# Optimization experiments

Hardware: AMD Instinct MI355X
Metric: run time of the kernel (lower is better)

Reference implementation:

```python
import jax, jax.numpy as jnp
import numpy as np
import math

NHEADS = 8


def pos_encoding_2d(d_model, H, W):
    dm = d_model // 2
    div = jnp.exp(jnp.arange(0, dm, 2, dtype=jnp.float32) * (-math.log(10000.0) / dm))  # [dm//2]
    pw = jnp.arange(W, dtype=jnp.float32)[:, None] * div  # [W, dm//2]
    ph = jnp.arange(H, dtype=jnp.float32)[:, None] * div  # [H, dm//2]
    pe = jnp.zeros((d_model, H, W), jnp.float32)
    pe = pe.at[0:dm:2].set(jnp.broadcast_to(jnp.sin(pw).T[:, None, :], (dm // 2, H, W)))
    pe = pe.at[1:dm:2].set(jnp.broadcast_to(jnp.cos(pw).T[:, None, :], (dm // 2, H, W)))
    pe = pe.at[dm::2].set(jnp.broadcast_to(jnp.sin(ph).T[:, :, None], (dm // 2, H, W)))
    pe = pe.at[dm + 1::2].set(jnp.broadcast_to(jnp.cos(ph).T[:, :, None], (dm // 2, H, W)))
    return pe


def conv_same(x, w, b):
    y = jax.lax.conv_general_dilated(x, w, (1, 1), 'SAME',
                                     dimension_numbers=('NCHW', 'OIHW', 'NCHW'))
    return y + b[None, :, None, None]


def layernorm(x, g, b, eps=1e-5):
    mu = x.mean(-1, keepdims=True)
    var = ((x - mu) ** 2).mean(-1, keepdims=True)
    return (x - mu) / jnp.sqrt(var + eps) * g + b


def setup_inputs() -> dict:
    key = jax.random.key(0)
    B, C, H, W = 8, 256, 32, 32
    KQV, NH, K = 64, NHEADS, 3
    ks = jax.random.split(key, 16)
    s_conv = 1.0 / math.sqrt(C * K * K)
    s_lin = 1.0 / math.sqrt(NH * KQV)
    s_ff = 1.0 / math.sqrt(C)
    return {
        'x': jax.random.normal(ks[0], (B, C, H, W), jnp.float32),
        'Wk': jax.random.normal(ks[1], (NH * KQV, C, K, K), jnp.float32) * s_conv,
        'bk': jax.random.normal(ks[2], (NH * KQV,), jnp.float32) * s_conv,
        'Wq': jax.random.normal(ks[3], (NH * KQV, C, K, K), jnp.float32) * s_conv,
        'bq': jax.random.normal(ks[4], (NH * KQV,), jnp.float32) * s_conv,
        'Wv': jax.random.normal(ks[5], (NH * KQV, C, K, K), jnp.float32) * s_conv,
        'bv': jax.random.normal(ks[6], (NH * KQV,), jnp.float32) * s_conv,
        'Wproj': jax.random.normal(ks[7], (C, NH * KQV), jnp.float32) * s_lin,
        'bproj': jax.random.normal(ks[8], (C,), jnp.float32) * s_lin,
        'ln_g': jnp.ones((C,), jnp.float32),
        'ln_b': jnp.zeros((C,), jnp.float32),
        'W1': jax.random.normal(ks[9], (C, C), jnp.float32) * s_ff,
        'b1': jax.random.normal(ks[10], (C,), jnp.float32) * s_ff,
        'W2': jax.random.normal(ks[11], (C, C), jnp.float32) * s_ff,
        'b2': jax.random.normal(ks[12], (C,), jnp.float32) * s_ff,
    }


def reference(x, Wk, bk, Wq, bq, Wv, bv, Wproj, bproj, ln_g, ln_b, W1, b1, W2, b2):
    B, C, H, W = x.shape
    N = H * W
    pe = pos_encoding_2d(C, H, W)
    xp = x + pe[None]                                   # [B,C,H,W]
    xflat = xp.reshape(B, C, N).transpose(0, 2, 1)      # [B,N,C]

    def heads(w, b):
        return conv_same(xp, w, b).reshape(B, NHEADS, -1, N)  # [B,h,c,N]

    k = heads(Wk, bk)
    q = heads(Wq, bq)
    v = heads(Wv, bv)
    scores = jnp.einsum('bhcn,bhcm->bhnm', k, q) / N    # K^T Q / N, [B,h,N,N]
    sm = jax.nn.softmax(scores, axis=1)                 # Softmax2d -> over HEAD dim (faithful)
    att = jnp.einsum('bhnm,bhcm->bhnc', sm, v)          # [B,h,N,c]
    att = att.transpose(0, 2, 3, 1).reshape(B, N, -1)   # [B,N,c*h] (channel-major, head-minor)
    attproj = att @ Wproj.T + bproj                     # [B,N,C]
    addnormed = layernorm(xflat + attproj, ln_g, ln_b)
    h1 = addnormed @ W1.T + b1
    h1 = jnp.where(h1 > 0, h1, 0.1 * h1)                # LeakyReLU(0.1)
    h2 = h1 @ W2.T + b2
    out = layernorm(h2 + addnormed, ln_g, ln_b)         # same LN params reused (faithful)
    return out.transpose(0, 2, 1).reshape(B, C, H, W)
```

## Files before the change

### kernel.cpp

```cpp
#include <hip/hip_runtime.h>
#include <stdint.h>

typedef __attribute__((ext_vector_type(8))) short short8;
typedef __attribute__((ext_vector_type(4))) short s16x4;
typedef __attribute__((ext_vector_type(4))) float f32x4;

#define DEVI __device__ __forceinline__

#if __has_builtin(__builtin_amdgcn_mfma_f32_16x16x16_bf16)
#define MFMA16(a, b, c) __builtin_amdgcn_mfma_f32_16x16x16_bf16(a, b, c, 0, 0, 0)
#else
#define MFMA16(a, b, c) __builtin_amdgcn_mfma_f32_16x16x16bf16_1k(a, b, c, 0, 0, 0)
#endif

DEVI unsigned short f2bf(float f) {
  union { float f; uint32_t u; } v; v.f = f;
  return (unsigned short)((v.u + 0x7fffu + ((v.u >> 16) & 1u)) >> 16);
}

DEVI float bf2f(uint32_t hi16) {
  union { uint32_t u; float f; } v; v.u = hi16;
  return v.f;
}

DEVI uint32_t pkbf(float a, float b) {
  union { float f; uint32_t u; } x, y; x.f = a; y.f = b;
  return ((x.u + 0x8000u) >> 16) | (((y.u + 0x8000u) >> 16) << 16);
}

DEVI void gload_lds16(const void* g, void* l) {
  __builtin_amdgcn_global_load_lds(
      (const __attribute__((address_space(1))) uint32_t*)g,
      (__attribute__((address_space(3))) uint32_t*)l, 16, 0, 0);
}

__global__ __launch_bounds__(256) void k_xpt(const float* __restrict__ x,
                                             const float* __restrict__ T,
                                             unsigned short* __restrict__ xpt_bf,
                                             float* __restrict__ xpt_f) {
  __shared__ __align__(16) float tile[32][36];
  const int b = blockIdx.z, c0 = blockIdx.x * 32, n0 = blockIdx.y * 32;
  const int t = threadIdx.x;
  {
    const int cl = t >> 3, ng = (t & 7) * 4;
    const int c = c0 + cl;
    float4 v = *(const float4*)(x + ((size_t)b * 256 + c) * 1024 + n0 + ng);
    float p0, p1, p2, p3;
    if (c < 128) {
      p0 = T[c * 32 + ng + 0]; p1 = T[c * 32 + ng + 1];
      p2 = T[c * 32 + ng + 2]; p3 = T[c * 32 + ng + 3];
    } else {
      p0 = p1 = p2 = p3 = T[c * 32 + (n0 >> 5)];
    }
    tile[ng + 0][cl] = v.x + p0;
    tile[ng + 1][cl] = v.y + p1;
    tile[ng + 2][cl] = v.z + p2;
    tile[ng + 3][cl] = v.w + p3;
  }
  __syncthreads();
  {
    const int nl = t >> 3, cg = (t & 7) * 4;
    float o0 = tile[nl][cg + 0], o1 = tile[nl][cg + 1];
    float o2 = tile[nl][cg + 2], o3 = tile[nl][cg + 3];
    size_t row = (size_t)b * 1024 + n0 + nl;
    *(float4*)(xpt_f + row * 256 + c0 + cg) = make_float4(o0, o1, o2, o3);
    uint32_t lo = (uint32_t)f2bf(o0) | ((uint32_t)f2bf(o1) << 16);
    uint32_t hi = (uint32_t)f2bf(o2) | ((uint32_t)f2bf(o3) << 16);
    *(uint2*)(xpt_bf + row * 256 + c0 + cg) = make_uint2(lo, hi);
  }
}

__global__ void k_prep(const float* __restrict__ Wk, const float* __restrict__ Wq,
                       const float* __restrict__ Wv, const float* __restrict__ bk,
                       const float* __restrict__ bq, const float* __restrict__ bv,
                       const float* __restrict__ Wproj, const float* __restrict__ W1,
                       const float* __restrict__ W2, unsigned short* __restrict__ Wpack,
                       float* __restrict__ bias_kqv, unsigned short* __restrict__ WprojP,
                       unsigned short* __restrict__ W1b, unsigned short* __restrict__ W2b,
                       float* __restrict__ T, float* __restrict__ zp) {
  int bid = blockIdx.x;
  if (bid < 13824) {
    int i = bid * 256 + threadIdx.x;
    if (i >= 1536 * 2304) return;
    int o = i / 2304, kn = i % 2304;
    int ci = kn & 255, khw = kn >> 8;
    const float* src = (o < 512) ? Wk : ((o < 1024) ? Wq : Wv);
    int oo = o & 511;
    Wpack[i] = f2bf(src[((size_t)oo * 256 + ci) * 9 + khw]);
  } else if (bid < 14336) {
    int i = (bid - 13824) * 256 + threadIdx.x;
    if (i < 1536)
      bias_kqv[i] = (i < 512) ? bk[i] : ((i < 1024) ? bq[i - 512] : bv[i - 1024]);
    {
      int j = i >> 9, f = i & 511;
      int h = f >> 6, c = f & 63;
      unsigned short v = f2bf(Wproj[(size_t)j * 512 + c * 8 + h]);
      WprojP[(size_t)j * 1024 + f] = v;
      WprojP[(size_t)j * 1024 + 512 + f] = v;
    }
    if (i < 65536) {
      W1b[i] = f2bf(W1[i]);
      W2b[i] = f2bf(W2[i]);
    }
  } else {
    int c = threadIdx.x;
    zp[c] = 0.0f;
    int idx = ((c >= 128) ? c - 128 : c) >> 1;
    float freq = expf(-(float)idx * (logf(10000.0f) / 64.0f));
    for (int p = 0; p < 32; ++p) {
      float ang = (float)p * freq;
      T[c * 32 + p] = (c & 1) ? cosf(ang) : sinf(ang);
    }
  }
}

__global__ __launch_bounds__(256, 2) void k_gemm_conv(const unsigned short* __restrict__ xpt,
                                                      const unsigned short* __restrict__ Wp,
                                                      unsigned short* __restrict__ kqv,
                                                      const float* __restrict__ bias,
                                                      const char* __restrict__ zp) {
  __shared__ __align__(16) unsigned short As[2][128 * 64];
  __shared__ __align__(16) unsigned short Bs[2][192 * 64];
  const int tid = threadIdx.x, l = tid & 63, w = tid >> 6;
  const int wm = w >> 1, wn = w & 1, g = l >> 4, ln = l & 15;
  const int id = blockIdx.x + (blockIdx.y << 6);
  const int nid = ((id & 7) << 6) + (id >> 3);
  const int m0 = (nid & 63) * 128, n0 = (nid >> 6) * 192;
  const int swz = (l & 7) ^ (l >> 3);

  const char* pAbase[4];
#pragma unroll
  for (int j = 0; j < 4; ++j) {
    int r = m0 + (w * 4 + j) * 8 + (l >> 3);
    pAbase[j] = (const char*)xpt + ((size_t)r * 256 + swz * 8) * 2;
  }
  const char* pB0 = (const char*)Wp +
                    ((size_t)(n0 + w * 48 + (l >> 3)) * 2304 + swz * 8) * 2;

  f32x4 acc[4][6] = {};
  int vmask = 0;
  int aoff = 0;

  auto setTap = [&](int tap) {
    int d3 = (tap * 11) >> 5;
    int dy = d3 - 1, dx = tap - d3 * 3 - 1;
    aoff = (dy * 32 + dx) * 512;
    int m = 0;
#pragma unroll
    for (int j = 0; j < 4; ++j) {
      int r = m0 + (w * 4 + j) * 8 + (l >> 3);
      int y = ((r >> 5) & 31) + dy;
      int x = (r & 31) + dx;
      if (((unsigned)y < 32u) && ((unsigned)x < 32u)) m |= (1 << j);
    }
    vmask = m;
  };

  auto STAGE = [&](int buf, int kb) {
#pragma unroll
    for (int j = 0; j < 4; ++j) {
      const char* a = (vmask & (1 << j)) ? (pAbase[j] + aoff) : zp;
      gload_lds16(a, (char*)As + buf * 16384 + (w * 4 + j) * 1024);
    }
#pragma unroll
    for (int j = 0; j < 6; ++j) {
      gload_lds16(pB0 + j * 36864 + kb, (char*)Bs + buf * 24576 + (w * 6 + j) * 1024);
    }
  };

  auto COMPUTE = [&](int buf) {
    const char* Ab2 = (const char*)As + buf * 16384;
    const char* Bb2 = (const char*)Bs + buf * 24576;
#pragma unroll
    for (int kk = 0; kk < 2; ++kk) {
      short8 af[4], bfr[6];
#pragma unroll
      for (int fm = 0; fm < 4; ++fm)
        af[fm] = *(const short8*)(Ab2 + (wm * 64 + fm * 16 + ln) * 128 +
                                  (((kk * 4 + g) ^ (ln & 7)) * 16));
#pragma unroll
      for (int fn = 0; fn < 6; ++fn)
        bfr[fn] = *(const short8*)(Bb2 + (wn * 96 + fn * 16 + ln) * 128 +
                                   (((kk * 4 + g) ^ (ln & 7)) * 16));
#pragma unroll
      for (int fm = 0; fm < 4; ++fm)
#pragma unroll
        for (int fn = 0; fn < 6; ++fn)
          acc[fm][fn] = __builtin_amdgcn_mfma_f32_16x16x32_bf16(af[fm], bfr[fn], acc[fm][fn], 0, 0, 0);
    }
  };

  setTap(0);
  STAGE(0, 0);
  aoff += 128;
  int kb = 128;
  for (int s = 0; s < 36; ++s) {
    const int buf = s & 1;
    if (s < 35) {
      if (((s + 1) & 3) == 0) setTap((s + 1) >> 2);
      STAGE(buf ^ 1, kb);
      kb += 128;
      aoff += 128;
      asm volatile("s_waitcnt vmcnt(10)" ::: "memory");
    } else {
      asm volatile("s_waitcnt vmcnt(0)" ::: "memory");
    }
    __builtin_amdgcn_s_barrier();
    __builtin_amdgcn_sched_barrier(0);
    COMPUTE(buf);
    asm volatile("s_waitcnt lgkmcnt(0)" ::: "memory");
    __builtin_amdgcn_s_barrier();
    __builtin_amdgcn_sched_barrier(0);
  }

#pragma unroll
  for (int fm = 0; fm < 4; ++fm)
#pragma unroll
    for (int fn = 0; fn < 6; ++fn) {
      int col = n0 + wn * 96 + fn * 16 + ln;
      float bb = bias[col];
#pragma unroll
      for (int r = 0; r < 4; ++r) {
        int row = m0 + wm * 64 + fm * 16 + g * 4 + r;
        kqv[(size_t)row * 1536 + col] = f2bf(acc[fm][fn][r] + bb);
      }
    }
}

__global__ __launch_bounds__(512, 4) void k_attn(const unsigned short* __restrict__ kqv,
                                                 unsigned short* __restrict__ part) {
  __shared__ __align__(16) unsigned short Qs[16][512];
  __shared__ __align__(16) char VsRaw[2][32 * 544];
  __shared__ __align__(16) float sums[4][2][64][4];
  const int tid = threadIdx.x, l = tid & 63, w = tid >> 6;
  const int g = l >> 4, ln = l & 15;
  const int nt = w & 1, hg = w >> 1;
  const int id = blockIdx.x;
  const int b = id & 7, ng = (id >> 3) & 31, ch = id >> 8;
  const int n0 = ng * 32 + nt * 16;
  const int m_base = ch * 512;
  const size_t rowBase = (size_t)b * 1024;
  const float SC = 1.0f / 1024.0f;

  short8 ak[2][2];
#pragma unroll
  for (int hl = 0; hl < 2; ++hl)
#pragma unroll
    for (int kk = 0; kk < 2; ++kk)
      ak[hl][kk] = *(const short8*)&kqv[(rowBase + n0 + ln) * 1536 +
                                        (hg * 2 + hl) * 64 + kk * 32 + g * 8];

  f32x4 acc[2][4] = {};

  const int r0 = w * 2, r1 = w * 2 + 1;
  const char* pRow = (const char*)kqv +
                     (size_t)(rowBase + m_base + r0) * 3072 + 1024 + (size_t)l * 16;
  uint4 q0, q1, v0, v1;

  auto LOADREGS = [&]() {
    q0 = *(const uint4*)pRow;
    v0 = *(const uint4*)(pRow + 1024);
    q1 = *(const uint4*)(pRow + 3072);
    v1 = *(const uint4*)(pRow + 4096);
    pRow += 49152;
  };
  char* const dQ0 = (char*)Qs + r0 * 1024 + ((l ^ (r0 & 7)) * 16);
  char* const dQ1 = (char*)Qs + r1 * 1024 + ((l ^ (r1 & 7)) * 16);
  const uint32_t vOff = (uint32_t)(l >> 1) * 544 + (uint32_t)(l & 1) * 16;
  auto DSW = [&](int vbuf) {
    *(uint4*)dQ0 = q0;
    *(uint4*)dQ1 = q1;
    char* vb = VsRaw[vbuf];
    *(uint4*)(vb + vOff + r0 * 32) = v0;
    *(uint4*)(vb + vOff + r1 * 32) = v1;
  };

  LOADREGS();
  asm volatile("s_waitcnt vmcnt(0)" ::: "memory");
  DSW(0);
  asm volatile("s_waitcnt lgkmcnt(0)" ::: "memory");
  __builtin_amdgcn_s_barrier();
  __builtin_amdgcn_sched_barrier(0);

  for (int s = 0; s < 32; ++s) {
    const int buf = s & 1;
    if (s < 31) LOADREGS();

    f32x4 sv[2] = {};
    __builtin_amdgcn_s_setprio(1);
#pragma unroll
    for (int kk = 0; kk < 2; ++kk)
#pragma unroll
      for (int hl = 0; hl < 2; ++hl) {
        int chq = (hg * 2 + hl) * 8 + kk * 4 + g;
        short8 qa = *(const short8*)((const char*)Qs + ln * 1024 +
                                     ((chq ^ (ln & 7)) * 16));
        sv[hl] = __builtin_amdgcn_mfma_f32_16x16x32_bf16(qa, ak[hl][kk], sv[hl], 0, 0, 0);
      }
    __builtin_amdgcn_s_setprio(0);

    f32x4 e0, e1, ps;
#pragma unroll
    for (int j = 0; j < 4; ++j) {
      e0[j] = __expf(sv[0][j] * SC);
      e1[j] = __expf(sv[1][j] * SC);
      ps[j] = e0[j] + e1[j];
    }
    *(f32x4*)&sums[hg][nt][l][0] = ps;
    asm volatile("s_waitcnt lgkmcnt(0)" ::: "memory");
    __builtin_amdgcn_s_barrier();
    __builtin_amdgcn_sched_barrier(0);

    f32x4 tot = ps;
#pragma unroll
    for (int d = 1; d < 4; ++d) {
      f32x4 o = *(const f32x4*)&sums[(hg + d) & 3][nt][l][0];
      tot[0] += o[0]; tot[1] += o[1]; tot[2] += o[2]; tot[3] += o[3];
    }
    f32x4 inv;
#pragma unroll
    for (int j = 0; j < 4; ++j) inv[j] = __builtin_amdgcn_rcpf(tot[j]);

    const uint32_t vsB = (uint32_t)(uintptr_t)VsRaw[buf] + l * 8;
    s16x4 vf[8];
#pragma unroll
    for (int hl = 0; hl < 2; ++hl) {
      uint32_t ah = vsB + (hg * 2 + hl) * 2176;
      asm volatile("ds_read_b64_tr_b16 %0, %1" : "=v"(vf[hl * 4 + 0]) : "v"(ah));
      asm volatile("ds_read_b64_tr_b16 %0, %1 offset:544" : "=v"(vf[hl * 4 + 1]) : "v"(ah));
      asm volatile("ds_read_b64_tr_b16 %0, %1 offset:1088" : "=v"(vf[hl * 4 + 2]) : "v"(ah));
      asm volatile("ds_read_b64_tr_b16 %0, %1 offset:1632" : "=v"(vf[hl * 4 + 3]) : "v"(ah));
    }
    asm volatile("s_waitcnt lgkmcnt(0)" ::: "memory");
    __builtin_amdgcn_sched_barrier(0);
    union { uint32_t u[2]; s16x4 v4; } pc0, pc1;
    pc0.u[0] = pkbf(e0[0] * inv[0], e0[1] * inv[1]);
    pc0.u[1] = pkbf(e0[2] * inv[2], e0[3] * inv[3]);
    pc1.u[0] = pkbf(e1[0] * inv[0], e1[1] * inv[1]);
    pc1.u[1] = pkbf(e1[2] * inv[2], e1[3] * inv[3]);
    __builtin_amdgcn_s_setprio(1);
#pragma unroll
    for (int cf = 0; cf < 4; ++cf) {
      acc[0][cf] = MFMA16(vf[cf], pc0.v4, acc[0][cf]);
      acc[1][cf] = MFMA16(vf[4 + cf], pc1.v4, acc[1][cf]);
    }
    __builtin_amdgcn_s_setprio(0);

    if (s < 31) {
      asm volatile("s_waitcnt vmcnt(0)" ::: "memory");
      DSW(buf ^ 1);
    }
    asm volatile("s_waitcnt lgkmcnt(0)" ::: "memory");
    __builtin_amdgcn_s_barrier();
    __builtin_amdgcn_sched_barrier(0);
  }

  const size_t outBase = (size_t)ch * 8192 * 512 + (rowBase + n0 + ln) * 512;
#pragma unroll
  for (int hl = 0; hl < 2; ++hl)
#pragma unroll
    for (int cf = 0; cf < 4; ++cf)
#pragma unroll
      for (int r2 = 0; r2 < 2; ++r2) {
        int c = (hg * 2 + hl) * 64 + cf * 16 + g * 4 + r2 * 2;
        uint32_t u = (uint32_t)f2bf(acc[hl][cf][2 * r2]) |
                     ((uint32_t)f2bf(acc[hl][cf][2 * r2 + 1]) << 16);
        *(uint32_t*)&part[outBase + c] = u;
      }
}

__global__ __launch_bounds__(256) void k_projffn1(const unsigned short* __restrict__ part,
                                                  const unsigned short* __restrict__ Wp,
                                                  const float* __restrict__ bias,
                                                  const float* __restrict__ resid,
                                                  const float* __restrict__ lg,
                                                  const float* __restrict__ lb,
                                                  float* __restrict__ addnf,
                                                  const unsigned short* __restrict__ W1b,
                                                  const float* __restrict__ b1,
                                                  unsigned short* __restrict__ h1) {
  __shared__ __align__(16) unsigned short As[32 * 64];
  __shared__ __align__(16) unsigned short Bs[256 * 64];
  __shared__ __align__(16) unsigned short As2[32 * 256];
  __shared__ float rsum[4][32][2];
  const int tid = threadIdx.x, l = tid & 63, w = tid >> 6;
  const int g4 = l >> 4, ln = l & 15;
  const int m0 = blockIdx.x * 32;
  const int swz = (l & 7) ^ (l >> 3);
  f32x4 acc[2][4] = {};

  for (int kt = 0; kt < 1024; kt += 64) {
    gload_lds16((const char*)part + (((size_t)(kt >> 9) * 8192 * 512) +
                                     (size_t)(m0 + w * 8 + (l >> 3)) * 512 +
                                     (kt & 511) + swz * 8) * 2,
                (char*)As + w * 1024);
#pragma unroll
    for (int j = 0; j < 8; ++j) {
      int seg = w * 8 + j;
      gload_lds16((const char*)Wp + ((size_t)(seg * 8 + (l >> 3)) * 1024 + kt + swz * 8) * 2,
                  (char*)Bs + seg * 1024);
    }
    __syncthreads();
#pragma unroll
    for (int kk = 0; kk < 2; ++kk) {
      short8 af[2], bfr[4];
#pragma unroll
      for (int fm = 0; fm < 2; ++fm)
        af[fm] = *(const short8*)((const char*)As + (fm * 16 + ln) * 128 +
                                  (((kk * 4 + g4) ^ (ln & 7)) * 16));
#pragma unroll
      for (int fn = 0; fn < 4; ++fn)
        bfr[fn] = *(const short8*)((const char*)Bs + (w * 64 + fn * 16 + ln) * 128 +
                                   (((kk * 4 + g4) ^ (ln & 7)) * 16));
#pragma unroll
      for (int fm = 0; fm < 2; ++fm)
#pragma unroll
        for (int fn = 0; fn < 4; ++fn)
          acc[fm][fn] = __builtin_amdgcn_mfma_f32_16x16x32_bf16(af[fm], bfr[fn], acc[fm][fn], 0, 0, 0);
    }
    __syncthreads();
  }

  float vals[2][4][4];
#pragma unroll
  for (int fm = 0; fm < 2; ++fm)
#pragma unroll
    for (int r = 0; r < 4; ++r) {
      int row_l = fm * 16 + g4 * 4 + r;
      float s = 0.f, q = 0.f;
#pragma unroll
      for (int fn = 0; fn < 4; ++fn) {
        int col = w * 64 + fn * 16 + ln;
        float v = acc[fm][fn][r] + bias[col] + resid[(size_t)(m0 + row_l) * 256 + col];
        vals[fm][fn][r] = v;
        s += v;
        q += v * v;
      }
#pragma unroll
      for (int o = 1; o < 16; o <<= 1) {
        s += __shfl_xor(s, o, 64);
        q += __shfl_xor(q, o, 64);
      }
      if (ln == 0) {
        rsum[w][row_l][0] = s;
        rsum[w][row_l][1] = q;
      }
    }
  __syncthreads();

#pragma unroll
  for (int fm = 0; fm < 2; ++fm)
#pragma unroll
    for (int r = 0; r < 4; ++r) {
      int row_l = fm * 16 + g4 * 4 + r;
      float s = rsum[0][row_l][0] + rsum[1][row_l][0] + rsum[2][row_l][0] + rsum[3][row_l][0];
      float q = rsum[0][row_l][1] + rsum[1][row_l][1] + rsum[2][row_l][1] + rsum[3][row_l][1];
      float mu = s * (1.0f / 256.0f);
      float rstd = rsqrtf(q * (1.0f / 256.0f) - mu * mu + 1e-5f);
      size_t rowOff = (size_t)(m0 + row_l) * 256;
#pragma unroll
      for (int fn = 0; fn < 4; ++fn) {
        int col = w * 64 + fn * 16 + ln;
        float o = (vals[fm][fn][r] - mu) * rstd * lg[col] + lb[col];
        addnf[rowOff + col] = o;
        int chunk = col >> 3;
        int slot = chunk ^ (row_l & 7);
        *(unsigned short*)((char*)As2 + row_l * 512 + slot * 16 + (col & 7) * 2) = f2bf(o);
      }
    }
  __syncthreads();

  f32x4 acc2[2][4] = {};
  for (int kt = 0; kt < 256; kt += 64) {
#pragma unroll
    for (int j = 0; j < 8; ++j) {
      int seg = w * 8 + j;
      gload_lds16((const char*)W1b + ((size_t)(seg * 8 + (l >> 3)) * 256 + kt + swz * 8) * 2,
                  (char*)Bs + seg * 1024);
    }
    __syncthreads();
#pragma unroll
    for (int kk = 0; kk < 2; ++kk) {
      short8 af[2], bfr[4];
#pragma unroll
      for (int fm = 0; fm < 2; ++fm) {
        int row = fm * 16 + ln;
        int chunk = (kt >> 3) + kk * 4 + g4;
        af[fm] = *(const short8*)((const char*)As2 + row * 512 +
                                  ((chunk ^ (row & 7)) * 16));
      }
#pragma unroll
      for (int fn = 0; fn < 4; ++fn)
        bfr[fn] = *(const short8*)((const char*)Bs + (w * 64 + fn * 16 + ln) * 128 +
                                   (((kk * 4 + g4) ^ (ln & 7)) * 16));
#pragma unroll
      for (int fm = 0; fm < 2; ++fm)
#pragma unroll
        for (int fn = 0; fn < 4; ++fn)
          acc2[fm][fn] = __builtin_amdgcn_mfma_f32_16x16x32_bf16(af[fm], bfr[fn], acc2[fm][fn], 0, 0, 0);
    }
    __syncthreads();
  }

#pragma unroll
  for (int fm = 0; fm < 2; ++fm)
#pragma unroll
    for (int fn = 0; fn < 4; ++fn)
#pragma unroll
      for (int r = 0; r < 4; ++r) {
        int row = m0 + fm * 16 + g4 * 4 + r;
        int col = w * 64 + fn * 16 + ln;
        float v = acc2[fm][fn][r] + b1[col];
        v = (v > 0.f) ? v : 0.1f * v;
        h1[(size_t)row * 256 + col] = f2bf(v);
      }
}

__global__ __launch_bounds__(256) void k_ffn2out(const unsigned short* __restrict__ h1,
                                                 const unsigned short* __restrict__ W2b,
                                                 const float* __restrict__ b2,
                                                 const float* __restrict__ addnf,
                                                 const float* __restrict__ lg,
                                                 const float* __restrict__ lb,
                                                 float* __restrict__ out) {
  __shared__ __align__(16) unsigned short As[32 * 64];
  __shared__ __align__(16) unsigned short Bs[256 * 64];
  __shared__ __align__(16) float Tt[256][33];
  __shared__ float rsum[4][32][2];
  const int tid = threadIdx.x, l = tid & 63, w = tid >> 6;
  const int g4 = l >> 4, ln = l & 15;
  const int m0 = blockIdx.x * 32;
  const int swz = (l & 7) ^ (l >> 3);
  f32x4 acc[2][4] = {};

  for (int kt = 0; kt < 256; kt += 64) {
    gload_lds16((const char*)h1 + ((size_t)(m0 + w * 8 + (l >> 3)) * 256 + kt + swz * 8) * 2,
                (char*)As + w * 1024);
#pragma unroll
    for (int j = 0; j < 8; ++j) {
      int seg = w * 8 + j;
      gload_lds16((const char*)W2b + ((size_t)(seg * 8 + (l >> 3)) * 256 + kt + swz * 8) * 2,
                  (char*)Bs + seg * 1024);
    }
    __syncthreads();
#pragma unroll
    for (int kk = 0; kk < 2; ++kk) {
      short8 af[2], bfr[4];
#pragma unroll
      for (int fm = 0; fm < 2; ++fm)
        af[fm] = *(const short8*)((const char*)As + (fm * 16 + ln) * 128 +
                                  (((kk * 4 + g4) ^ (ln & 7)) * 16));
#pragma unroll
      for (int fn = 0; fn < 4; ++fn)
        bfr[fn] = *(const short8*)((const char*)Bs + (w * 64 + fn * 16 + ln) * 128 +
                                   (((kk * 4 + g4) ^ (ln & 7)) * 16));
#pragma unroll
      for (int fm = 0; fm < 2; ++fm)
#pragma unroll
        for (int fn = 0; fn < 4; ++fn)
          acc[fm][fn] = __builtin_amdgcn_mfma_f32_16x16x32_bf16(af[fm], bfr[fn], acc[fm][fn], 0, 0, 0);
    }
    __syncthreads();
  }

  float vals[2][4][4];
#pragma unroll
  for (int fm = 0; fm < 2; ++fm)
#pragma unroll
    for (int r = 0; r < 4; ++r) {
      int row_l = fm * 16 + g4 * 4 + r;
      float s = 0.f, q = 0.f;
#pragma unroll
      for (int fn = 0; fn < 4; ++fn) {
        int col = w * 64 + fn * 16 + ln;
        float v = acc[fm][fn][r] + b2[col] + addnf[(size_t)(m0 + row_l) * 256 + col];
        vals[fm][fn][r] = v;
        s += v;
        q += v * v;
      }
#pragma unroll
      for (int o = 1; o < 16; o <<= 1) {
        s += __shfl_xor(s, o, 64);
        q += __shfl_xor(q, o, 64);
      }
      if (ln == 0) {
        rsum[w][row_l][0] = s;
        rsum[w][row_l][1] = q;
      }
    }
  __syncthreads();

#pragma unroll
  for (int fm = 0; fm < 2; ++fm)
#pragma unroll
    for (int r = 0; r < 4; ++r) {
      int row_l = fm * 16 + g4 * 4 + r;
      float s = rsum[0][row_l][0] + rsum[1][row_l][0] + rsum[2][row_l][0] + rsum[3][row_l][0];
      float q = rsum[0][row_l][1] + rsum[1][row_l][1] + rsum[2][row_l][1] + rsum[3][row_l][1];
      float mu = s * (1.0f / 256.0f);
      float rstd = rsqrtf(q * (1.0f / 256.0f) - mu * mu + 1e-5f);
#pragma unroll
      for (int fn = 0; fn < 4; ++fn) {
        int col = w * 64 + fn * 16 + ln;
        Tt[col][row_l] = (vals[fm][fn][r] - mu) * rstd * lg[col] + lb[col];
      }
    }
  __syncthreads();

  const int bimg = m0 >> 10, nn0 = m0 & 1023;
#pragma unroll
  for (int i = 0; i < 8; ++i) {
    int c = i * 32 + (tid >> 3);
    int ng = (tid & 7) * 4;
    float4 o = make_float4(Tt[c][ng], Tt[c][ng + 1], Tt[c][ng + 2], Tt[c][ng + 3]);
    *(float4*)&out[((size_t)bimg * 256 + c) * 1024 + nn0 + ng] = o;
  }
}

extern "C" void kernel_launch(void* const* d_in, const int* in_sizes, int n_in,
                              void* d_out, int out_size, void* d_ws, size_t ws_size,
                              hipStream_t stream) {
  const float* x     = (const float*)d_in[0];
  const float* Wk    = (const float*)d_in[1];
  const float* bk    = (const float*)d_in[2];
  const float* Wq    = (const float*)d_in[3];
  const float* bq    = (const float*)d_in[4];
  const float* Wv    = (const float*)d_in[5];
  const float* bv    = (const float*)d_in[6];
  const float* Wproj = (const float*)d_in[7];
  const float* bproj = (const float*)d_in[8];
  const float* ln_g  = (const float*)d_in[9];
  const float* ln_b  = (const float*)d_in[10];
  const float* W1    = (const float*)d_in[11];
  const float* b1    = (const float*)d_in[12];
  const float* W2    = (const float*)d_in[13];
  const float* b2    = (const float*)d_in[14];

  char* ws = (char*)d_ws;
  constexpr size_t OFF_XPTB  = 0;
  constexpr size_t OFF_XPTF  = OFF_XPTB  + (size_t)8192 * 256 * 2;
  constexpr size_t OFF_WPACK = OFF_XPTF  + (size_t)8192 * 256 * 4;
  constexpr size_t OFF_BIAS  = OFF_WPACK + (size_t)1536 * 2304 * 2;
  constexpr size_t OFF_WPROJ = OFF_BIAS  + (size_t)1536 * 4;
  constexpr size_t OFF_W1B   = OFF_WPROJ + (size_t)256 * 1024 * 2;
  constexpr size_t OFF_W2B   = OFF_W1B   + (size_t)256 * 256 * 2;
  constexpr size_t OFF_PET   = OFF_W2B   + (size_t)256 * 256 * 2;
  constexpr size_t OFF_ZERO  = OFF_PET   + (size_t)256 * 32 * 4;
  constexpr size_t OFF_KQV   = OFF_ZERO  + 1024;
  constexpr size_t OFF_PART  = OFF_KQV   + (size_t)8192 * 1536 * 2;
  constexpr size_t OFF_ADDNF = OFF_PART  + (size_t)2 * 8192 * 512 * 2;
  constexpr size_t OFF_H1    = OFF_ADDNF + (size_t)8192 * 256 * 4;

  (void)in_sizes; (void)n_in; (void)out_size; (void)ws_size;

  const char* zp = (const char*)(ws + OFF_ZERO);

  k_prep<<<14337, 256, 0, stream>>>(Wk, Wq, Wv, bk, bq, bv, Wproj, W1, W2,
                                    (unsigned short*)(ws + OFF_WPACK),
                                    (float*)(ws + OFF_BIAS),
                                    (unsigned short*)(ws + OFF_WPROJ),
                                    (unsigned short*)(ws + OFF_W1B),
                                    (unsigned short*)(ws + OFF_W2B),
                                    (float*)(ws + OFF_PET), (float*)(ws + OFF_ZERO));
  k_xpt<<<dim3(8, 32, 8), 256, 0, stream>>>(x, (const float*)(ws + OFF_PET),
                                            (unsigned short*)(ws + OFF_XPTB),
                                            (float*)(ws + OFF_XPTF));
  k_gemm_conv<<<dim3(64, 8), 256, 0, stream>>>(
      (const unsigned short*)(ws + OFF_XPTB), (const unsigned short*)(ws + OFF_WPACK),
      (unsigned short*)(ws + OFF_KQV), (const float*)(ws + OFF_BIAS), zp);
  k_attn<<<dim3(512), 512, 0, stream>>>((const unsigned short*)(ws + OFF_KQV),
                                        (unsigned short*)(ws + OFF_PART));
  k_projffn1<<<256, 256, 0, stream>>>((const unsigned short*)(ws + OFF_PART),
                                      (const unsigned short*)(ws + OFF_WPROJ), bproj,
                                      (const float*)(ws + OFF_XPTF), ln_g, ln_b,
                                      (float*)(ws + OFF_ADDNF),
                                      (const unsigned short*)(ws + OFF_W1B), b1,
                                      (unsigned short*)(ws + OFF_H1));
  k_ffn2out<<<256, 256, 0, stream>>>((const unsigned short*)(ws + OFF_H1),
                                     (const unsigned short*)(ws + OFF_W2B), b2,
                                     (const float*)(ws + OFF_ADDNF), ln_g, ln_b,
                                     (float*)d_out);
}
```

Measured before the change: 181.8 us.

## Fuse FFN2 and output layernorm into projection kernel; tweak conv/attn scheduling

Merges the proj+LN+FFN1 kernel and the FFN2+LN+transpose kernel into a single k_tail kernel. The LayerNorm output and the LeakyReLU h1 stay in registers and LDS instead of round-tripping through global memory, and one launch is removed. The shared-memory buffer for the W2 tile is aliased with the transpose buffer. The change also raises wave priority around the conv GEMM MFMA block and moves the softmax-denominator reduction after the V transpose-reads are issued, so LDS latency overlaps with that arithmetic. The cost is more LDS per block in the fused kernel, which may lower occupancy.

```diff
diff --git a/kernel.cpp b/kernel.cpp
--- a/kernel.cpp
+++ b/kernel.cpp
@@ -171,6 +171,7 @@
   auto COMPUTE = [&](int buf) {
     const char* Ab2 = (const char*)As + buf * 16384;
     const char* Bb2 = (const char*)Bs + buf * 24576;
+    __builtin_amdgcn_s_setprio(1);
 #pragma unroll
     for (int kk = 0; kk < 2; ++kk) {
       short8 af[4], bfr[6];
@@ -188,6 +189,7 @@
         for (int fn = 0; fn < 6; ++fn)
           acc[fm][fn] = __builtin_amdgcn_mfma_f32_16x16x32_bf16(af[fm], bfr[fn], acc[fm][fn], 0, 0, 0);
     }
+    __builtin_amdgcn_s_setprio(0);
   };
 
   setTap(0);
@@ -311,16 +313,6 @@
     __builtin_amdgcn_s_barrier();
     __builtin_amdgcn_sched_barrier(0);
 
-    f32x4 tot = ps;
-#pragma unroll
-    for (int d = 1; d < 4; ++d) {
-      f32x4 o = *(const f32x4*)&sums[(hg + d) & 3][nt][l][0];
-      tot[0] += o[0]; tot[1] += o[1]; tot[2] += o[2]; tot[3] += o[3];
-    }
-    f32x4 inv;
-#pragma unroll
-    for (int j = 0; j < 4; ++j) inv[j] = __builtin_amdgcn_rcpf(tot[j]);
-
     const uint32_t vsB = (uint32_t)(uintptr_t)VsRaw[buf] + l * 8;
     s16x4 vf[8];
 #pragma unroll
@@ -331,6 +323,17 @@
       asm volatile("ds_read_b64_tr_b16 %0, %1 offset:1088" : "=v"(vf[hl * 4 + 2]) : "v"(ah));
       asm volatile("ds_read_b64_tr_b16 %0, %1 offset:1632" : "=v"(vf[hl * 4 + 3]) : "v"(ah));
     }
+
+    f32x4 tot = ps;
+#pragma unroll
+    for (int d = 1; d < 4; ++d) {
+      f32x4 o = *(const f32x4*)&sums[(hg + d) & 3][nt][l][0];
+      tot[0] += o[0]; tot[1] += o[1]; tot[2] += o[2]; tot[3] += o[3];
+    }
+    f32x4 inv;
+#pragma unroll
+    for (int j = 0; j < 4; ++j) inv[j] = __builtin_amdgcn_rcpf(tot[j]);
+
     asm volatile("s_waitcnt lgkmcnt(0)" ::: "memory");
     __builtin_amdgcn_sched_barrier(0);
     union { uint32_t u[2]; s16x4 v4; } pc0, pc1;
@@ -369,26 +372,30 @@
       }
 }
 
-__global__ __launch_bounds__(256) void k_projffn1(const unsigned short* __restrict__ part,
-                                                  const unsigned short* __restrict__ Wp,
-                                                  const float* __restrict__ bias,
-                                                  const float* __restrict__ resid,
-                                                  const float* __restrict__ lg,
-                                                  const float* __restrict__ lb,
-                                                  float* __restrict__ addnf,
-                                                  const unsigned short* __restrict__ W1b,
-                                                  const float* __restrict__ b1,
-                                                  unsigned short* __restrict__ h1) {
+__global__ __launch_bounds__(256) void k_tail(const unsigned short* __restrict__ part,
+                                              const unsigned short* __restrict__ Wp,
+                                              const float* __restrict__ bproj,
+                                              const float* __restrict__ resid,
+                                              const float* __restrict__ lg,
+                                              const float* __restrict__ lb,
+                                              const unsigned short* __restrict__ W1b,
+                                              const float* __restrict__ b1,
+                                              const unsigned short* __restrict__ W2b,
+                                              const float* __restrict__ b2,
+                                              float* __restrict__ out) {
   __shared__ __align__(16) unsigned short As[32 * 64];
-  __shared__ __align__(16) unsigned short Bs[256 * 64];
+  __shared__ __align__(16) char BsTt[33792];
   __shared__ __align__(16) unsigned short As2[32 * 256];
+  __shared__ __align__(16) unsigned short H1s[32 * 256];
   __shared__ float rsum[4][32][2];
+  unsigned short* const Bs = (unsigned short*)BsTt;
+  float(* const Tt)[33] = (float(*)[33])BsTt;
   const int tid = threadIdx.x, l = tid & 63, w = tid >> 6;
   const int g4 = l >> 4, ln = l & 15;
   const int m0 = blockIdx.x * 32;
   const int swz = (l & 7) ^ (l >> 3);
+
   f32x4 acc[2][4] = {};
-
   for (int kt = 0; kt < 1024; kt += 64) {
     gload_lds16((const char*)part + (((size_t)(kt >> 9) * 8192 * 512) +
                                      (size_t)(m0 + w * 8 + (l >> 3)) * 512 +
@@ -431,7 +438,7 @@
 #pragma unroll
       for (int fn = 0; fn < 4; ++fn) {
         int col = w * 64 + fn * 16 + ln;
-        float v = acc[fm][fn][r] + bias[col] + resid[(size_t)(m0 + row_l) * 256 + col];
+        float v = acc[fm][fn][r] + bproj[col] + resid[(size_t)(m0 + row_l) * 256 + col];
         vals[fm][fn][r] = v;
         s += v;
         q += v * v;
@@ -457,14 +464,12 @@
       float q = rsum[0][row_l][1] + rsum[1][row_l][1] + rsum[2][row_l][1] + rsum[3][row_l][1];
       float mu = s * (1.0f / 256.0f);
       float rstd = rsqrtf(q * (1.0f / 256.0f) - mu * mu + 1e-5f);
-      size_t rowOff = (size_t)(m0 + row_l) * 256;
 #pragma unroll
       for (int fn = 0; fn < 4; ++fn) {
         int col = w * 64 + fn * 16 + ln;
         float o = (vals[fm][fn][r] - mu) * rstd * lg[col] + lb[col];
-        addnf[rowOff + col] = o;
-        int chunk = col >> 3;
-        int slot = chunk ^ (row_l & 7);
+        vals[fm][fn][r] = o;
+        int slot = (col >> 3) ^ (row_l & 7);
         *(unsigned short*)((char*)As2 + row_l * 512 + slot * 16 + (col & 7) * 2) = f2bf(o);
       }
     }
@@ -486,8 +491,7 @@
       for (int fm = 0; fm < 2; ++fm) {
         int row = fm * 16 + ln;
         int chunk = (kt >> 3) + kk * 4 + g4;
-        af[fm] = *(const short8*)((const char*)As2 + row * 512 +
-                                  ((chunk ^ (row & 7)) * 16));
+        af[fm] = *(const short8*)((const char*)As2 + row * 512 + ((chunk ^ (row & 7)) * 16));
       }
 #pragma unroll
       for (int fn = 0; fn < 4; ++fn)
@@ -501,41 +505,23 @@
     }
     __syncthreads();
   }
-
 #pragma unroll
   for (int fm = 0; fm < 2; ++fm)
 #pragma unroll
     for (int fn = 0; fn < 4; ++fn)
 #pragma unroll
       for (int r = 0; r < 4; ++r) {
-        int row = m0 + fm * 16 + g4 * 4 + r;
+        int row_l = fm * 16 + g4 * 4 + r;
         int col = w * 64 + fn * 16 + ln;
         float v = acc2[fm][fn][r] + b1[col];
         v = (v > 0.f) ? v : 0.1f * v;
-        h1[(size_t)row * 256 + col] = f2bf(v);
-      }
-}
-
-__global__ __launch_bounds__(256) void k_ffn2out(const unsigned short* __restrict__ h1,
-                                                 const unsigned short* __restrict__ W2b,
-                                                 const float* __restrict__ b2,
-                                                 const float* __restrict__ addnf,
-                                                 const float* __restrict__ lg,
-                                                 const float* __restrict__ lb,
-                                                 float* __restrict__ out) {
-  __shared__ __align__(16) unsigned short As[32 * 64];
-  __shared__ __align__(16) unsigned short Bs[256 * 64];
-  __shared__ __align__(16) float Tt[256][33];
-  __shared__ float rsum[4][32][2];
-  const int tid = threadIdx.x, l = tid & 63, w = tid >> 6;
-  const int g4 = l >> 4, ln = l & 15;
-  const int m0 = blockIdx.x * 32;
-  const int swz = (l & 7) ^ (l >> 3);
-  f32x4 acc[2][4] = {};
-
+        int slot = (col >> 3) ^ (row_l & 7);
+        *(unsigned short*)((char*)H1s + row_l * 512 + slot * 16 + (col & 7) * 2) = f2bf(v);
+      }
+  __syncthreads();
+
+  f32x4 acc3[2][4] = {};
   for (int kt = 0; kt < 256; kt += 64) {
-    gload_lds16((const char*)h1 + ((size_t)(m0 + w * 8 + (l >> 3)) * 256 + kt + swz * 8) * 2,
-                (char*)As + w * 1024);
 #pragma unroll
     for (int j = 0; j < 8; ++j) {
       int seg = w * 8 + j;
@@ -547,9 +533,11 @@
     for (int kk = 0; kk < 2; ++kk) {
       short8 af[2], bfr[4];
 #pragma unroll
-      for (int fm = 0; fm < 2; ++fm)
-        af[fm] = *(const short8*)((const char*)As + (fm * 16 + ln) * 128 +
-                                  (((kk * 4 + g4) ^ (ln & 7)) * 16));
+      for (int fm = 0; fm < 2; ++fm) {
+        int row = fm * 16 + ln;
+        int chunk = (kt >> 3) + kk * 4 + g4;
+        af[fm] = *(const short8*)((const char*)H1s + row * 512 + ((chunk ^ (row & 7)) * 16));
+      }
 #pragma unroll
       for (int fn = 0; fn < 4; ++fn)
         bfr[fn] = *(const short8*)((const char*)Bs + (w * 64 + fn * 16 + ln) * 128 +
@@ -558,12 +546,11 @@
       for (int fm = 0; fm < 2; ++fm)
 #pragma unroll
         for (int fn = 0; fn < 4; ++fn)
-          acc[fm][fn] = __builtin_amdgcn_mfma_f32_16x16x32_bf16(af[fm], bfr[fn], acc[fm][fn], 0, 0, 0);
+          acc3[fm][fn] = __builtin_amdgcn_mfma_f32_16x16x32_bf16(af[fm], bfr[fn], acc3[fm][fn], 0, 0, 0);
     }
     __syncthreads();
   }
 
-  float vals[2][4][4];
 #pragma unroll
   for (int fm = 0; fm < 2; ++fm)
 #pragma unroll
@@ -573,7 +560,7 @@
 #pragma unroll
       for (int fn = 0; fn < 4; ++fn) {
         int col = w * 64 + fn * 16 + ln;
-        float v = acc[fm][fn][r] + b2[col] + addnf[(size_t)(m0 + row_l) * 256 + col];
+        float v = acc3[fm][fn][r] + b2[col] + vals[fm][fn][r];
         vals[fm][fn][r] = v;
         s += v;
         q += v * v;
@@ -648,8 +635,6 @@
   constexpr size_t OFF_ZERO  = OFF_PET   + (size_t)256 * 32 * 4;
   constexpr size_t OFF_KQV   = OFF_ZERO  + 1024;
   constexpr size_t OFF_PART  = OFF_KQV   + (size_t)8192 * 1536 * 2;
-  constexpr size_t OFF_ADDNF = OFF_PART  + (size_t)2 * 8192 * 512 * 2;
-  constexpr size_t OFF_H1    = OFF_ADDNF + (size_t)8192 * 256 * 4;
 
   (void)in_sizes; (void)n_in; (void)out_size; (void)ws_size;
 
@@ -670,14 +655,10 @@
       (unsigned short*)(ws + OFF_KQV), (const float*)(ws + OFF_BIAS), zp);
   k_attn<<<dim3(512), 512, 0, stream>>>((const unsigned short*)(ws + OFF_KQV),
                                         (unsigned short*)(ws + OFF_PART));
-  k_projffn1<<<256, 256, 0, stream>>>((const unsigned short*)(ws + OFF_PART),
-                                      (const unsigned short*)(ws + OFF_WPROJ), bproj,
-                                      (const float*)(ws + OFF_XPTF), ln_g, ln_b,
-                                      (float*)(ws + OFF_ADDNF),
-                                      (const unsigned short*)(ws + OFF_W1B), b1,
-                                      (unsigned short*)(ws + OFF_H1));
-  k_ffn2out<<<256, 256, 0, stream>>>((const unsigned short*)(ws + OFF_H1),
-                                     (const unsigned short*)(ws + OFF_W2B), b2,
-                                     (const float*)(ws + OFF_ADDNF), ln_g, ln_b,
-                                     (float*)d_out);
-}
+  k_tail<<<256, 256, 0, stream>>>((const unsigned short*)(ws + OFF_PART),
+                                  (const unsigned short*)(ws + OFF_WPROJ), bproj,
+                                  (const float*)(ws + OFF_XPTF), ln_g, ln_b,
+                                  (const unsigned short*)(ws + OFF_W1B), b1,
+                                  (const unsigned short*)(ws + OFF_W2B), b2,
+                                  (float*)d_out);
+}
```

After: 173.1 us. -4.8%, faster.
